# Optimization experiments

Hardware: AMD Instinct MI355X
Metric: run time of the kernel (lower is better)

Reference implementation:

```python
import jax, jax.numpy as jnp
import numpy as np

N_NODES = 10000
N_EDGES = 160000


def _conv2d(x, w, b):
    y = jax.lax.conv_general_dilated(x, w, (1, 1), 'SAME',
                                     dimension_numbers=('NCHW', 'OIHW', 'NCHW'))
    return jax.nn.selu(y + b[None, :, None, None])


def _cnn(cf, cnn_w1, cnn_b1, cnn_w2, cnn_b2, cnn_w3, cnn_b3, cnn_w4, cnn_b4):
    h = _conv2d(cf, cnn_w1, cnn_b1)
    h = _conv2d(h, cnn_w2, cnn_b2)
    h = _conv2d(h, cnn_w3, cnn_b3)
    h = _conv2d(h, cnn_w4, cnn_b4)
    return h.mean(axis=(2, 3))  # (1, 24) global avg pool


def _gat(x, src, dst, W, a_s, a_d, b, n):
    # PyG GATConv, concat=False (mean over heads), add_self_loops handled by caller
    H, C = a_s.shape
    h = (x @ W).reshape(-1, H, C)                      # (N,H,C)
    e = jax.nn.leaky_relu((h * a_s).sum(-1)[src] +
                          (h * a_d).sum(-1)[dst], 0.2)  # (E,H)
    m = jax.ops.segment_max(e, dst, num_segments=n)
    p = jnp.exp(e - m[dst])
    z = jax.ops.segment_sum(p, dst, num_segments=n)
    alpha = p / (z[dst] + 1e-16)
    out = jax.ops.segment_sum(h[src] * alpha[..., None], dst, num_segments=n)
    return out.mean(axis=1) + b


def _fix_boundary(v, up, down, left, right):
    c0 = jnp.where(down, 0.0, jnp.where(up, 1.0, v[:, 0]))
    c1 = jnp.where(right, 1.0, jnp.where(left, 0.0, v[:, 1]))
    return v.at[:, 0].set(c0).at[:, 1].set(c1)


def setup_inputs() -> dict:
    key = jax.random.key(0)
    ks = jax.random.split(key, 40)
    d = {}
    d['x'] = jax.random.uniform(ks[0], (N_NODES, 10), dtype=jnp.float32)
    d['edge_index'] = jax.random.randint(ks[1], (2, N_EDGES), 0, N_NODES, dtype=jnp.int64)
    d['conv_feat'] = jax.random.normal(ks[2], (1, 4, 64, 64), dtype=jnp.float32)
    cnn_dims = [(16, 4), (32, 16), (64, 32), (24, 64)]
    for i, (o, c) in enumerate(cnn_dims, 1):
        d[f'cnn_w{i}'] = jax.random.normal(ks[2 + i], (o, c, 3, 3), jnp.float32) * 0.1
        d[f'cnn_b{i}'] = jnp.zeros((o,), jnp.float32)
    gat_dims = [(34, 8, 64), (64, 16, 128), (128, 8, 256), (256, 8, 128), (128, 16, 2)]
    for i, (fin, H, C) in enumerate(gat_dims, 1):
        k1, k2, k3 = jax.random.split(ks[10 + i], 3)
        d[f'g{i}_w'] = jax.random.normal(k1, (fin, H * C), jnp.float32) * 0.1
        d[f'g{i}_as'] = jax.random.normal(k2, (H, C), jnp.float32) * 0.1
        d[f'g{i}_ad'] = jax.random.normal(k3, (H, C), jnp.float32) * 0.1
        d[f'g{i}_b'] = jnp.zeros((C,), jnp.float32)
    return d


def reference(x, edge_index, conv_feat,
              cnn_w1, cnn_b1, cnn_w2, cnn_b2, cnn_w3, cnn_b3, cnn_w4, cnn_b4,
              g1_w, g1_as, g1_ad, g1_b,
              g2_w, g2_as, g2_ad, g2_b,
              g3_w, g3_as, g3_ad, g3_b,
              g4_w, g4_as, g4_ad, g4_b,
              g5_w, g5_as, g5_ad, g5_b):
    n = x.shape[0]
    # boundary masks from raw node coordinates
    up, down = x[:, 0] == 1, x[:, 0] == 0
    left, right = x[:, 1] == 0, x[:, 1] == 1
    # add self loops (PyG GATConv default)
    loops = jnp.arange(n, dtype=edge_index.dtype)
    src = jnp.concatenate([edge_index[0], loops])
    dst = jnp.concatenate([edge_index[1], loops])

    gfeat = _cnn(conv_feat, cnn_w1, cnn_b1, cnn_w2, cnn_b2, cnn_w3, cnn_b3, cnn_w4, cnn_b4)
    h = jnp.concatenate([jnp.broadcast_to(gfeat, (n, gfeat.shape[1])), x], axis=1)

    h = jax.nn.selu(_gat(h, src, dst, g1_w, g1_as, g1_ad, g1_b, n))
    h = _fix_boundary(h, up, down, left, right)
    h = jax.nn.selu(_gat(h, src, dst, g2_w, g2_as, g2_ad, g2_b, n))
    h = _fix_boundary(h, up, down, left, right)
    h = jax.nn.selu(_gat(h, src, dst, g3_w, g3_as, g3_ad, g3_b, n))
    h = _fix_boundary(h, up, down, left, right)
    h = jax.nn.selu(_gat(h, src, dst, g4_w, g4_as, g4_ad, g4_b, n))
    h = _fix_boundary(h, up, down, left, right)
    res = jax.nn.selu(_gat(h, src, dst, g5_w, g5_as, g5_ad, g5_b, n))
    out = x[:, :2] + res
    out = _fix_boundary(out, up, down, left, right)
    return out
```

## Files before the change

kernel.cpp:

```cpp
#include <hip/hip_runtime.h>
#include <hip/hip_fp16.h>
#include <math.h>


#define DEVFN static __device__ __forceinline__

typedef __attribute__((ext_vector_type(8))) _Float16 half8;
typedef __attribute__((ext_vector_type(4))) _Float16 half4v;
typedef __attribute__((ext_vector_type(4))) float f32x4;

DEVFN float selu_f(float v) {
    const float scale = 1.0507009873554805f;
    const float alpha = 1.6732632423543772f;
    return v > 0.f ? scale * v : scale * alpha * (expf(v) - 1.f);
}

DEVFN float lrelu02(float v) { return v > 0.f ? v : 0.2f * v; }

#define PST 66
#define PSZ (66 * 66)

__global__ __launch_bounds__(256) void conv3x3_first(const float* __restrict__ cf,
                                                     const float* __restrict__ w,
                                                     const float* __restrict__ b,
                                                     float* __restrict__ out) {
    int x  = threadIdx.x & 63;
    int yg = threadIdx.x >> 6;
    int y  = blockIdx.x * 4 + yg;
    int co = blockIdx.y;
    float acc = b[co];
    const float* wp = w + (size_t)co * 4 * 9;
#pragma unroll
    for (int ci = 0; ci < 4; ++ci) {
        const float* ip = cf + ci * 4096;
        const float* wr = wp + ci * 9;
#pragma unroll
        for (int ky = 0; ky < 3; ++ky) {
            int yy = y + ky - 1;
            if (yy < 0 || yy >= 64) continue;
#pragma unroll
            for (int kx = 0; kx < 3; ++kx) {
                int xx = x + kx - 1;
                if (xx < 0 || xx >= 64) continue;
                acc += wr[ky * 3 + kx] * ip[yy * 64 + xx];
            }
        }
    }
    out[(size_t)co * PSZ + (y + 1) * PST + (x + 1)] = selu_f(acc);
}

template <int CIN>
__global__ __launch_bounds__(256) void conv3x3_pad(const float* __restrict__ in,
                                                   const float* __restrict__ w,
                                                   const float* __restrict__ b,
                                                   float* __restrict__ out) {
    int x  = threadIdx.x & 63;
    int yg = threadIdx.x >> 6;
    int y  = blockIdx.x * 4 + yg;
    int co = blockIdx.y;
    float acc = b[co];
    const float* wp = w + (size_t)co * CIN * 9;
#pragma unroll 4
    for (int ci = 0; ci < CIN; ++ci) {
        const float* ip = in + ci * PSZ + y * PST + x;
        const float* wr = wp + ci * 9;
        acc += wr[0] * ip[0]           + wr[1] * ip[1]           + wr[2] * ip[2]
             + wr[3] * ip[PST]         + wr[4] * ip[PST + 1]     + wr[5] * ip[PST + 2]
             + wr[6] * ip[2 * PST]     + wr[7] * ip[2 * PST + 1] + wr[8] * ip[2 * PST + 2];
    }
    out[(size_t)co * PSZ + (y + 1) * PST + (x + 1)] = selu_f(acc);
}

__global__ void avgpool_c(const float* __restrict__ in, float* __restrict__ gfeat) {
    int c = blockIdx.x;
    int t = threadIdx.x;
    float s = 0.f;
    for (int i = t; i < 4096; i += 256) {
        int y = i >> 6, x = i & 63;
        s += in[c * PSZ + (y + 1) * PST + (x + 1)];
    }
#pragma unroll
    for (int off = 32; off >= 1; off >>= 1) s += __shfl_xor(s, off);
    __shared__ float red[4];
    int wave = t >> 6, lane = t & 63;
    if (lane == 0) red[wave] = s;
    __syncthreads();
    if (t == 0) gfeat[c] = (red[0] + red[1] + red[2] + red[3]) * (1.f / 4096.f);
}

__global__ void build_h0(const float* __restrict__ x, const float* __restrict__ gfeat,
                         const float* __restrict__ we0,
                         __half* __restrict__ h0f, unsigned* __restrict__ masks,
                         float* __restrict__ esed, int N) {
    int n = blockIdx.x * blockDim.x + threadIdx.x;
    if (n >= N) return;
    float x0 = x[n * 10 + 0], x1 = x[n * 10 + 1];
    unsigned mk = (x0 == 1.f ? 1u : 0u) | (x0 == 0.f ? 2u : 0u) |
                  (x1 == 0.f ? 4u : 0u) | (x1 == 1.f ? 8u : 0u);
    masks[n] = mk;
    __half* hq = h0f + (size_t)n * 64;
    float hf[64];
#pragma unroll
    for (int j = 0; j < 64; ++j) {
        float v = (j < 24) ? gfeat[j] : (j < 34 ? x[n * 10 + (j - 24)] : 0.f);
        __half hv = __float2half(v);
        hq[j] = hv;
        hf[j] = __half2float(hv);
    }
    float s[16];
#pragma unroll
    for (int o = 0; o < 16; ++o) s[o] = 0.f;
    for (int k = 0; k < 64; ++k) {
        float f = hf[k];
        const float* wk = we0 + k * 16;
#pragma unroll
        for (int o = 0; o < 16; ++o) s[o] += f * wk[o];
    }
#pragma unroll
    for (int o = 0; o < 16; ++o) esed[(size_t)n * 16 + o] = s[o];
}

__global__ void count_dst(const int* __restrict__ ei, int* __restrict__ cnt, int E, int N) {
    int t = blockIdx.x * blockDim.x + threadIdx.x;
    if (t >= E + N) return;
    int dst = (t < E) ? ei[E + t] : (t - E);
    atomicAdd(&cnt[dst], 1);
}

__global__ __launch_bounds__(1024) void scan_all(const int* __restrict__ cnt,
                                                 int* __restrict__ indptr,
                                                 int* __restrict__ cursor,
                                                 int n, int total) {
    __shared__ int sdata[1024];
    int t = threadIdx.x;
    int base = t * 10;
    int loc[10];
    int s = 0;
#pragma unroll
    for (int i = 0; i < 10; ++i) {
        int idx = base + i;
        int v = (idx < n) ? cnt[idx] : 0;
        loc[i] = s;
        s += v;
    }
    sdata[t] = s;
    __syncthreads();
    for (int off = 1; off < 1024; off <<= 1) {
        int tmp = (t >= off) ? sdata[t - off] : 0;
        __syncthreads();
        sdata[t] += tmp;
        __syncthreads();
    }
    int excl = (t == 0) ? 0 : sdata[t - 1];
#pragma unroll
    for (int i = 0; i < 10; ++i) {
        int idx = base + i;
        if (idx < n) {
            int e = excl + loc[i];
            indptr[idx] = e;
            cursor[idx] = e;
        }
    }
    if (t == 0) indptr[n] = total;
}

__global__ void scatter_edges(const int* __restrict__ ei, int* __restrict__ cursor,
                              int* __restrict__ col, int E, int N) {
    int t = blockIdx.x * blockDim.x + threadIdx.x;
    if (t >= E + N) return;
    int src, dst;
    if (t < E) { src = ei[t]; dst = ei[E + t]; }
    else       { src = dst = t - E; }
    int pos = atomicAdd(&cursor[dst], 1);
    col[pos] = src;
}

__global__ __launch_bounds__(256) void prep_all(
        const float* __restrict__ W0, const float* __restrict__ W1,
        const float* __restrict__ W2, const float* __restrict__ W3,
        const float* __restrict__ W4,
        const float* __restrict__ as0, const float* __restrict__ as1,
        const float* __restrict__ as2, const float* __restrict__ as3,
        const float* __restrict__ as4,
        const float* __restrict__ ad0, const float* __restrict__ ad1,
        const float* __restrict__ ad2, const float* __restrict__ ad3,
        const float* __restrict__ ad4,
        unsigned short* __restrict__ bt, float* __restrict__ wesed,
        float* __restrict__ wcomb) {
    const int Kc[5]  = {34, 64, 128, 256, 128};
    const int Kpc[5] = {64, 64, 128, 256, 128};
    const int Hc[5]  = {8, 16, 8, 8, 16};
    const int Cc[5]  = {64, 128, 256, 128, 2};
    const int HCc[5] = {512, 2048, 2048, 1024, 32};
    const int KAc[5] = {512, 1024, 1024, 2048, 2048};
    const int btOff[5] = {0, 32768, 163840, 425984, 0};
    const int weOff[5] = {0, 1024, 3072, 5120, 9216};

    int b = blockIdx.x, tid = threadIdx.x;

    if (b < 168) {
        int lyr, tloc;
        if (b < 8)        { lyr = 0; tloc = b; }
        else if (b < 40)  { lyr = 1; tloc = b - 8; }
        else if (b < 104) { lyr = 2; tloc = b - 40; }
        else              { lyr = 3; tloc = b - 104; }
        const int ktl[4] = {1, 1, 2, 4};
        const int mtl[4] = {1, 2, 4, 2};
        int kt = ktl[lyr], mt = mtl[lyr];
        int per_h = kt * mt;
        int h = tloc / per_h, r = tloc - h * per_h;
        int ki = r % kt, mi = r / kt;
        int k0 = ki * 64, m0 = mi * 64;
        int K = Kc[lyr], Kp = Kpc[lyr], C = Cc[lyr], HC = HCc[lyr], KA = KAc[lyr];
        const float* W;
        if (lyr == 0) W = W0; else if (lyr == 1) W = W1;
        else if (lyr == 2) W = W2; else W = W3;

        __shared__ float tile[64][65];
        int c = tid & 63, rg = tid >> 6;
        for (int r2 = rg; r2 < 64; r2 += 4) {
            int k = k0 + r2, m = m0 + c;
            float v = (k < K && m < C) ? W[(size_t)k * HC + h * C + m] : 0.f;
            tile[r2][c] = v;
        }
        __syncthreads();
        unsigned short* bp = bt + btOff[lyr];
        for (int mr = rg; mr < 64; mr += 4) {
            int m = m0 + mr, k = k0 + c;
            if (m < C && k < Kp)
                bp[(size_t)m * KA + h * Kp + k] =
                    __half_as_ushort(__float2half(tile[c][mr]));
        }
    } else if (b < 200) {
        int u = (b - 168) * 256 + tid;
        int k = u >> 6, o = u & 63;
        float s;
        if (o < 32) {
            int h = (o < 16) ? o : o - 16;
            const float* av = ((o < 16) ? as4 : ad4) + h * 2;
            s = W4[k * 32 + h * 2 + 0] * av[0] + W4[k * 32 + h * 2 + 1] * av[1];
        } else {
            s = W4[k * 32 + (o - 32)];
        }
        wcomb[u] = s;
    } else {
        int wb = b - 200;
        int lyr, u0;
        if (wb < 4)       { lyr = 0; u0 = wb * 256; }
        else if (wb < 12) { lyr = 1; u0 = (wb - 4) * 256; }
        else if (wb < 20) { lyr = 2; u0 = (wb - 12) * 256; }
        else if (wb < 36) { lyr = 3; u0 = (wb - 20) * 256; }
        else              { lyr = 4; u0 = (wb - 36) * 256; }
        int u = u0 + tid;
        int K = Kc[lyr], Kp = Kpc[lyr], H = Hc[lyr], C = Cc[lyr], HC = HCc[lyr];
        int H2 = 2 * H;
        if (u < Kp * H2) {
            int k = u / H2, o = u - k * H2;
            float s = 0.f;
            if (k < K) {
                int h = (o < H) ? o : o - H;
                const float *W, *as_, *ad_;
                if (lyr == 0)      { W = W0; as_ = as0; ad_ = ad0; }
                else if (lyr == 1) { W = W1; as_ = as1; ad_ = ad1; }
                else if (lyr == 2) { W = W2; as_ = as2; ad_ = ad2; }
                else if (lyr == 3) { W = W3; as_ = as3; ad_ = ad3; }
                else               { W = W4; as_ = as4; ad_ = ad4; }
                const float* av = ((o < H) ? as_ : ad_) + h * C;
                const float* wp = W + (size_t)k * HC + h * C;
#pragma unroll 4
                for (int c2 = 0; c2 < C; ++c2) s += wp[c2] * av[c2];
            }
            wesed[weOff[lyr] + u] = s;
        }
    }
}

template <int H, int KP, int CH, int NPB, int TWO>
__global__ __launch_bounds__(NPB * (KP / CH)) void gat_fused_lds(
        const __half* __restrict__ hinf, const float* __restrict__ esed,
        const float* __restrict__ esed2,
        const int* __restrict__ indptr, const int* __restrict__ col,
        __half* __restrict__ g, int N) {
    const int TPN = KP / CH;
    const int EC  = TPN / H;
    const int H2  = 2 * H;
    __shared__ float lds_p[NPB][2][TPN];
    int sub = threadIdx.x / TPN;
    int j   = threadIdx.x % TPN;
    int n = blockIdx.x * NPB + sub;
    if (n >= N) return;
    int e_my = j / H, h_my = j % H;
    int c0 = j * CH;
    float edv = esed[n * H2 + H + h_my];
    if constexpr (TWO) edv += esed2[n * H2 + H + h_my];

    float acc[H][CH];
#pragma unroll
    for (int h = 0; h < H; ++h)
#pragma unroll
        for (int t = 0; t < CH; ++t) acc[h][t] = 0.f;
    float zloc = 0.f;

    int beg = indptr[n], deg = indptr[n + 1] - beg;

    float p = 0.f;
    if (e_my < deg) {
        int srcm = col[beg + e_my];
        float es0 = esed[srcm * H2 + h_my];
        if constexpr (TWO) es0 += esed2[srcm * H2 + h_my];
        p = expf(lrelu02(es0 + edv));
    }
    int buf = 0;
    for (int base = 0; base < deg; base += EC) {
        zloc += p;
        lds_p[sub][buf][j] = p;
        __builtin_amdgcn_wave_barrier();
        int ce = base + EC + e_my;
        bool vnext = (ce < deg);
        float esv = 0.f;
        if (vnext) {
            int srcm = col[beg + ce];
            esv = esed[srcm * H2 + h_my];
            if constexpr (TWO) esv += esed2[srcm * H2 + h_my];
        }
#pragma unroll
        for (int e = 0; e < EC; ++e) {
            int idx = base + e;
            if (idx < deg) {
                int src = col[beg + idx];
                float f[CH];
                if (CH == 2) {
                    __half2 hv = *(const __half2*)(hinf + (size_t)src * KP + c0);
                    float2 ff = __half22float2(hv);
                    f[0] = ff.x; f[1] = ff.y;
                } else {
                    half4v hv = *(const half4v*)(hinf + (size_t)src * KP + c0);
                    f[0] = (float)hv[0]; f[1] = (float)hv[1];
                    f[2] = (float)hv[2]; f[3] = (float)hv[3];
                }
                const float4* ap = (const float4*)&lds_p[sub][buf][e * H];
#pragma unroll
                for (int q4 = 0; q4 < H / 4; ++q4) {
                    float4 a4 = ap[q4];
#pragma unroll
                    for (int t = 0; t < CH; ++t) {
                        acc[4 * q4 + 0][t] += a4.x * f[t];
                        acc[4 * q4 + 1][t] += a4.y * f[t];
                        acc[4 * q4 + 2][t] += a4.z * f[t];
                        acc[4 * q4 + 3][t] += a4.w * f[t];
                    }
                }
            }
        }
        p = vnext ? expf(lrelu02(esv + edv)) : 0.f;
        buf ^= 1;
    }

#pragma unroll
    for (int off = H; off < TPN; off <<= 1)
        zloc += __shfl_xor(zloc, off, TPN);
    float zinv_my = (1.f / H) / (zloc + 1e-16f);

    __half* gp = g + (size_t)n * (H * KP) + c0;
#pragma unroll
    for (int h = 0; h < H; ++h) {
        float zf = __shfl(zinv_my, h, TPN);
        if (CH == 2) {
            *(__half2*)(gp + h * KP) =
                __floats2half2_rn(acc[h][0] * zf, acc[h][1] * zf);
        } else {
            __half2 lo = __floats2half2_rn(acc[h][0] * zf, acc[h][1] * zf);
            __half2 hi = __floats2half2_rn(acc[h][2] * zf, acc[h][3] * zf);
            union { __half2 h2[2]; float2 f2; } u;
            u.h2[0] = lo; u.h2[1] = hi;
            *(float2*)(gp + h * KP) = u.f2;
        }
    }
}

template <int NPB>
__global__ __launch_bounds__(NPB * 32) void final_attn(
        const float* __restrict__ eyp, const int* __restrict__ indptr,
        const int* __restrict__ col, const float* __restrict__ b5,
        const unsigned* __restrict__ masks, const float* __restrict__ x,
        float* __restrict__ outp, int N) {
    int sub = threadIdx.x >> 5;
    int j   = threadIdx.x & 31;
    int n = blockIdx.x * NPB + sub;
    if (n >= N) return;
    int h = j >> 1;
    float edv = eyp[(size_t)n * 64 + 16 + h];
    int beg = indptr[n], end = indptr[n + 1];
    float z = 0.f, a = 0.f;
    int i = beg;
    for (; i + 1 < end; i += 2) {
        int s0 = col[i], s1 = col[i + 1];
        const float* r0 = eyp + (size_t)s0 * 64;
        const float* r1 = eyp + (size_t)s1 * 64;
        float es0 = r0[h], y0 = r0[32 + j];
        float es1 = r1[h], y1 = r1[32 + j];
        float p0 = expf(lrelu02(es0 + edv));
        float p1 = expf(lrelu02(es1 + edv));
        z += p0; a += p0 * y0;
        z += p1; a += p1 * y1;
    }
    for (; i < end; ++i) {
        const float* r = eyp + (size_t)col[i] * 64;
        float p = expf(lrelu02(r[h] + edv));
        z += p; a += p * r[32 + j];
    }
    float zf = (1.f / 16.f) / (z + 1e-16f);
    float val = a * zf;
#pragma unroll
    for (int off = 2; off <= 16; off <<= 1) val += __shfl_xor(val, off, 32);
    float other = __shfl_xor(val, 1, 32);
    if (j == 0) {
        unsigned mk = masks[n];
        float v0 = x[n * 10 + 0] + selu_f(val + b5[0]);
        float v1 = x[n * 10 + 1] + selu_f(other + b5[1]);
        if (mk & 2u) v0 = 0.f; else if (mk & 1u) v0 = 1.f;
        if (mk & 8u) v1 = 1.f; else if (mk & 4u) v1 = 0.f;
        outp[n * 2 + 0] = v0;
        outp[n * 2 + 1] = v1;
    }
}

#define LDP 72
template <int CW, int EOUT>
__global__ __launch_bounds__(256) void gemm16(const __half* __restrict__ A,
                                              const unsigned short* __restrict__ Bhi,
                                              const float* __restrict__ bias,
                                              const unsigned* __restrict__ masks,
                                              __half* __restrict__ O16,
                                              const float* __restrict__ wnext,
                                              float* __restrict__ eout,
                                              int N, int K, int M) {
    const int JT = CW / 64;
    const int BR = CW / 32;
    __shared__ __half lA[16 * LDP], lB[CW * LDP];
    __shared__ float vt[EOUT ? 16 : 1][EOUT ? (CW + 4) : 1];
    int tid = threadIdx.x;
    int wave = tid >> 6, lane = tid & 63;
    int ln16 = lane & 15, q = lane >> 4;
    int row0 = blockIdx.x * 16;
    int col0 = blockIdx.y * CW;
    int wc = wave * (CW / 4);

    int arow = tid >> 3;
    int ac   = (tid & 7) * 8;
    const __half* Bp = (const __half*)Bhi;
    const __half* ap = A + (size_t)min(row0 + arow, N - 1) * K + ac;
    const __half* bp[BR];
#pragma unroll
    for (int i = 0; i < BR; ++i)
        bp[i] = Bp + (size_t)(col0 + arow + 32 * i) * K + ac;

    half8 ra;
    if (tid < 128) ra = *(const half8*)(ap);
    half8 rb[BR];
#pragma unroll
    for (int i = 0; i < BR; ++i) rb[i] = *(const half8*)(bp[i]);

    f32x4 acc[JT];
#pragma unroll
    for (int j = 0; j < JT; ++j) acc[j] = (f32x4){0.f, 0.f, 0.f, 0.f};

    for (int kc = 0; kc < K; kc += 64) {
        __syncthreads();
        if (tid < 128) *(half8*)(lA + arow * LDP + ac) = ra;
#pragma unroll
        for (int i = 0; i < BR; ++i)
            *(half8*)(lB + (arow + 32 * i) * LDP + ac) = rb[i];
        __syncthreads();
        int kn = kc + 64;
        if (kn < K) {
            if (tid < 128) ra = *(const half8*)(ap + kn);
#pragma unroll
            for (int i = 0; i < BR; ++i) rb[i] = *(const half8*)(bp[i] + kn);
        }
#pragma unroll
        for (int kk = 0; kk < 2; ++kk) {
            half8 af = *(const half8*)(lA + ln16 * LDP + kk * 32 + q * 8);
#pragma unroll
            for (int j = 0; j < JT; ++j) {
                half8 bf = *(const half8*)(lB + (wc + j * 16 + ln16) * LDP + kk * 32 + q * 8);
                acc[j] = __builtin_amdgcn_mfma_f32_16x16x32_f16(af, bf, acc[j], 0, 0, 0);
            }
        }
    }

#pragma unroll
    for (int j = 0; j < JT; ++j) {
        int cc = col0 + wc + j * 16 + ln16;
        float bv = bias[cc];
#pragma unroll
        for (int r = 0; r < 4; ++r) {
            int rr = row0 + q * 4 + r;
            float v = selu_f(acc[j][r] + bv);
            if (cc < 2 && rr < N) {
                unsigned mk = masks[rr];
                if (cc == 0) { if (mk & 2u) v = 0.f; else if (mk & 1u) v = 1.f; }
                else         { if (mk & 8u) v = 1.f; else if (mk & 4u) v = 0.f; }
            }
            __half hv = __float2half(v);
            if (rr < N) O16[(size_t)rr * M + cc] = hv;
            if constexpr (EOUT > 0)
                vt[q * 4 + r][wc + j * 16 + ln16] = __half2float(hv);
        }
    }

    if constexpr (EOUT > 0) {
        __syncthreads();
        const int NG = 256 / EOUT;
        const int NI = 16 / NG;
        int o = tid & (EOUT - 1);
        int ngrp = tid / EOUT;
        const float* wp = wnext + (size_t)col0 * EOUT;
        float* ep = eout + (size_t)blockIdx.y * N * EOUT;
        float s[NI];
#pragma unroll
        for (int i = 0; i < NI; ++i) s[i] = 0.f;
        for (int k = 0; k < CW; ++k) {
            float wk = wp[k * EOUT + o];
#pragma unroll
            for (int i = 0; i < NI; ++i)
                s[i] += vt[ngrp + NG * i][k] * wk;
        }
#pragma unroll
        for (int i = 0; i < NI; ++i) {
            int n = row0 + ngrp + NG * i;
            if (n < N) ep[(size_t)n * EOUT + o] = s[i];
        }
    }
}

extern "C" void kernel_launch(void* const* d_in, const int* in_sizes, int n_in,
                              void* d_out, int out_size, void* d_ws, size_t ws_size,
                              hipStream_t stream) {
    const float* x   = (const float*)d_in[0];
    const int*   ei  = (const int*)d_in[1];
    const float* cf  = (const float*)d_in[2];
    const float* cw[4] = {(const float*)d_in[3], (const float*)d_in[5],
                          (const float*)d_in[7], (const float*)d_in[9]};
    const float* cb[4] = {(const float*)d_in[4], (const float*)d_in[6],
                          (const float*)d_in[8], (const float*)d_in[10]};
    const float* gw[5], *gas[5], *gad[5], *gb[5];
    for (int i = 0; i < 5; ++i) {
        gw[i]  = (const float*)d_in[11 + 4 * i];
        gas[i] = (const float*)d_in[12 + 4 * i];
        gad[i] = (const float*)d_in[13 + 4 * i];
        gb[i]  = (const float*)d_in[14 + 4 * i];
    }
    const int N = in_sizes[0] / 10;
    const int E = in_sizes[1] / 2;
    const int EN = E + N;

    char* base = (char*)d_ws;
    size_t off = 0;
    auto alloc = [&](size_t bytes) -> char* {
        char* p = base + off;
        off = (off + bytes + 255) & ~(size_t)255;
        return p;
    };
    float* c1p   = (float*)alloc((size_t)16 * PSZ * 4);
    float* c2p   = (float*)alloc((size_t)32 * PSZ * 4);
    float* c3p   = (float*)alloc((size_t)64 * PSZ * 4);
    float* c4p   = (float*)alloc((size_t)24 * PSZ * 4);
    float* gfeat = (float*)alloc(24 * 4);
    __half* hA16 = (__half*)alloc((size_t)N * 256 * 2);
    __half* hB16 = (__half*)alloc((size_t)N * 256 * 2);
    __half* g    = (__half*)alloc((size_t)N * 2048 * 2);
    float* esed  = (float*)alloc((size_t)N * 32 * 4);
    float* eyp   = (float*)alloc((size_t)N * 64 * 4);
    float* wesed = (float*)alloc((size_t)13312 * 4);
    float* wcomb = (float*)alloc((size_t)8192 * 4);
    unsigned short* bt = (unsigned short*)alloc((size_t)688128 * 2);
    unsigned* masks = (unsigned*)alloc((size_t)N * 4);
    int* cnt    = (int*)alloc((size_t)N * 4);
    int* indptr = (int*)alloc((size_t)(N + 1) * 4);
    int* cursor = (int*)alloc((size_t)N * 4);
    int* col    = (int*)alloc((size_t)EN * 4);
    (void)ws_size;

    prep_all<<<252, 256, 0, stream>>>(gw[0], gw[1], gw[2], gw[3], gw[4],
                                      gas[0], gas[1], gas[2], gas[3], gas[4],
                                      gad[0], gad[1], gad[2], gad[3], gad[4],
                                      bt, wesed, wcomb);

    hipMemsetAsync(c1p, 0, (size_t)136 * PSZ * 4, stream);
    conv3x3_first<<<dim3(16, 16), 256, 0, stream>>>(cf, cw[0], cb[0], c1p);
    conv3x3_pad<16><<<dim3(16, 32), 256, 0, stream>>>(c1p, cw[1], cb[1], c2p);
    conv3x3_pad<32><<<dim3(16, 64), 256, 0, stream>>>(c2p, cw[2], cb[2], c3p);
    conv3x3_pad<64><<<dim3(16, 24), 256, 0, stream>>>(c3p, cw[3], cb[3], c4p);
    avgpool_c<<<24, 256, 0, stream>>>(c4p, gfeat);

    build_h0<<<(N + 255) / 256, 256, 0, stream>>>(x, gfeat, wesed + 0, hA16, masks,
                                                  esed, N);

    hipMemsetAsync(cnt, 0, (size_t)N * 4, stream);
    count_dst<<<(EN + 255) / 256, 256, 0, stream>>>(ei, cnt, E, N);
    scan_all<<<1, 1024, 0, stream>>>(cnt, indptr, cursor, N, EN);
    scatter_edges<<<(EN + 255) / 256, 256, 0, stream>>>(ei, cursor, col, E, N);

    int gx16 = (N + 15) / 16;

    gat_fused_lds<8, 64, 4, 16, 0><<<(N + 15) / 16, 256, 0, stream>>>(
        hA16, esed, nullptr, indptr, col, g, N);
    gemm16<64, 32><<<dim3(gx16, 1), 256, 0, stream>>>(g, bt + 0, gb[0], masks, hB16,
                                                      wesed + 1024, esed, N, 512, 64);

    gat_fused_lds<16, 64, 2, 8, 0><<<(N + 7) / 8, 256, 0, stream>>>(
        hB16, esed, nullptr, indptr, col, g, N);
    gemm16<128, 16><<<dim3(gx16, 1), 256, 0, stream>>>(g, bt + 32768, gb[1], masks, hA16,
                                                       wesed + 3072, esed, N, 1024, 128);

    gat_fused_lds<8, 128, 4, 8, 0><<<(N + 7) / 8, 256, 0, stream>>>(
        hA16, esed, nullptr, indptr, col, g, N);
    gemm16<128, 16><<<dim3(gx16, 2), 256, 0, stream>>>(g, bt + 163840, gb[2], masks, hB16,
                                                       wesed + 5120, esed, N, 1024, 256);

    gat_fused_lds<8, 256, 4, 4, 1><<<(N + 3) / 4, 256, 0, stream>>>(
        hB16, esed, esed + (size_t)N * 16, indptr, col, g, N);
    gemm16<128, 64><<<dim3(gx16, 1), 256, 0, stream>>>(g, bt + 425984, gb[3], masks, hA16,
                                                       wcomb, eyp, N, 2048, 128);

    final_attn<8><<<(N + 7) / 8, 256, 0, stream>>>(eyp, indptr, col, gb[4],
                                                   masks, x, (float*)d_out, N);
}
```

Measured before the change: 429.0 us.

## Co-schedule CNN conv layers with CSR graph build in combined kernels

Merges the first three conv layers with the dst-count, scan and edge-scatter kernels into three combined launches whose block ranges split between the two independent jobs. The cnt buffer moves next to the conv buffers so a single memset clears both, dropping one memset and four launches. The scan now uses 256 threads with 40 elements each so it fits the 256-thread combined kernel. This serialises more work per scan thread and puts blocks with different register needs in one launch, which may lower occupancy for the conv blocks.

```diff
diff --git a/kernel.cpp b/kernel.cpp
--- a/kernel.cpp
+++ b/kernel.cpp
@@ -20,14 +20,12 @@
 #define PST 66
 #define PSZ (66 * 66)
 
-__global__ __launch_bounds__(256) void conv3x3_first(const float* __restrict__ cf,
-                                                     const float* __restrict__ w,
-                                                     const float* __restrict__ b,
-                                                     float* __restrict__ out) {
+DEVFN void conv_first_body(const float* __restrict__ cf, const float* __restrict__ w,
+                           const float* __restrict__ b, float* __restrict__ out,
+                           int bx, int co) {
     int x  = threadIdx.x & 63;
     int yg = threadIdx.x >> 6;
-    int y  = blockIdx.x * 4 + yg;
-    int co = blockIdx.y;
+    int y  = bx * 4 + yg;
     float acc = b[co];
     const float* wp = w + (size_t)co * 4 * 9;
 #pragma unroll
@@ -50,14 +48,12 @@
 }
 
 template <int CIN>
-__global__ __launch_bounds__(256) void conv3x3_pad(const float* __restrict__ in,
-                                                   const float* __restrict__ w,
-                                                   const float* __restrict__ b,
-                                                   float* __restrict__ out) {
+DEVFN void conv_pad_body(const float* __restrict__ in, const float* __restrict__ w,
+                         const float* __restrict__ b, float* __restrict__ out,
+                         int bx, int co) {
     int x  = threadIdx.x & 63;
     int yg = threadIdx.x >> 6;
-    int y  = blockIdx.x * 4 + yg;
-    int co = blockIdx.y;
+    int y  = bx * 4 + yg;
     float acc = b[co];
     const float* wp = w + (size_t)co * CIN * 9;
 #pragma unroll 4
@@ -69,6 +65,14 @@
              + wr[6] * ip[2 * PST]     + wr[7] * ip[2 * PST + 1] + wr[8] * ip[2 * PST + 2];
     }
     out[(size_t)co * PSZ + (y + 1) * PST + (x + 1)] = selu_f(acc);
+}
+
+template <int CIN>
+__global__ __launch_bounds__(256) void conv3x3_pad(const float* __restrict__ in,
+                                                   const float* __restrict__ w,
+                                                   const float* __restrict__ b,
+                                                   float* __restrict__ out) {
+    conv_pad_body<CIN>(in, w, b, out, blockIdx.x, blockIdx.y);
 }
 
 __global__ void avgpool_c(const float* __restrict__ in, float* __restrict__ gfeat) {
@@ -120,24 +124,23 @@
     for (int o = 0; o < 16; ++o) esed[(size_t)n * 16 + o] = s[o];
 }
 
-__global__ void count_dst(const int* __restrict__ ei, int* __restrict__ cnt, int E, int N) {
-    int t = blockIdx.x * blockDim.x + threadIdx.x;
+DEVFN void count_body(const int* __restrict__ ei, int* __restrict__ cnt,
+                      int blk, int E, int N) {
+    int t = blk * 256 + threadIdx.x;
     if (t >= E + N) return;
     int dst = (t < E) ? ei[E + t] : (t - E);
     atomicAdd(&cnt[dst], 1);
 }
 
-__global__ __launch_bounds__(1024) void scan_all(const int* __restrict__ cnt,
-                                                 int* __restrict__ indptr,
-                                                 int* __restrict__ cursor,
-                                                 int n, int total) {
-    __shared__ int sdata[1024];
+DEVFN void scan_body(const int* __restrict__ cnt, int* __restrict__ indptr,
+                     int* __restrict__ cursor, int n, int total) {
+    __shared__ int sdata[256];
     int t = threadIdx.x;
-    int base = t * 10;
-    int loc[10];
+    int base = t * 40;
+    int loc[40];
     int s = 0;
 #pragma unroll
-    for (int i = 0; i < 10; ++i) {
+    for (int i = 0; i < 40; ++i) {
         int idx = base + i;
         int v = (idx < n) ? cnt[idx] : 0;
         loc[i] = s;
@@ -145,7 +148,7 @@
     }
     sdata[t] = s;
     __syncthreads();
-    for (int off = 1; off < 1024; off <<= 1) {
+    for (int off = 1; off < 256; off <<= 1) {
         int tmp = (t >= off) ? sdata[t - off] : 0;
         __syncthreads();
         sdata[t] += tmp;
@@ -153,7 +156,7 @@
     }
     int excl = (t == 0) ? 0 : sdata[t - 1];
 #pragma unroll
-    for (int i = 0; i < 10; ++i) {
+    for (int i = 0; i < 40; ++i) {
         int idx = base + i;
         if (idx < n) {
             int e = excl + loc[i];
@@ -164,15 +167,56 @@
     if (t == 0) indptr[n] = total;
 }
 
-__global__ void scatter_edges(const int* __restrict__ ei, int* __restrict__ cursor,
-                              int* __restrict__ col, int E, int N) {
-    int t = blockIdx.x * blockDim.x + threadIdx.x;
+DEVFN void scatter_body(const int* __restrict__ ei, int* __restrict__ cursor,
+                        int* __restrict__ col, int blk, int E, int N) {
+    int t = blk * 256 + threadIdx.x;
     if (t >= E + N) return;
     int src, dst;
     if (t < E) { src = ei[t]; dst = ei[E + t]; }
     else       { src = dst = t - E; }
     int pos = atomicAdd(&cursor[dst], 1);
     col[pos] = src;
+}
+
+__global__ __launch_bounds__(256) void comboA(const float* __restrict__ cf,
+                                              const float* __restrict__ w0,
+                                              const float* __restrict__ b0,
+                                              float* __restrict__ c1p,
+                                              const int* __restrict__ ei,
+                                              int* __restrict__ cnt, int E, int N) {
+    int b = blockIdx.x;
+    if (b < 256) conv_first_body(cf, w0, b0, c1p, b % 16, b / 16);
+    else         count_body(ei, cnt, b - 256, E, N);
+}
+
+__global__ __launch_bounds__(256) void comboB(const int* __restrict__ cnt,
+                                              int* __restrict__ indptr,
+                                              int* __restrict__ cursor, int n, int total,
+                                              const float* __restrict__ c1p,
+                                              const float* __restrict__ w1,
+                                              const float* __restrict__ b1,
+                                              float* __restrict__ c2p) {
+    int b = blockIdx.x;
+    if (b == 0) scan_body(cnt, indptr, cursor, n, total);
+    else {
+        int blk = b - 1;
+        conv_pad_body<16>(c1p, w1, b1, c2p, blk % 16, blk / 16);
+    }
+}
+
+__global__ __launch_bounds__(256) void comboC(const int* __restrict__ ei,
+                                              int* __restrict__ cursor,
+                                              int* __restrict__ col, int E, int N, int CB,
+                                              const float* __restrict__ c2p,
+                                              const float* __restrict__ w2,
+                                              const float* __restrict__ b2,
+                                              float* __restrict__ c3p) {
+    int b = blockIdx.x;
+    if (b < CB) scatter_body(ei, cursor, col, b, E, N);
+    else {
+        int blk = b - CB;
+        conv_pad_body<32>(c2p, w2, b2, c3p, blk % 16, blk / 16);
+    }
 }
 
 __global__ __launch_bounds__(256) void prep_all(
@@ -554,6 +598,7 @@
     const int N = in_sizes[0] / 10;
     const int E = in_sizes[1] / 2;
     const int EN = E + N;
+    const int CB = (EN + 255) / 256;
 
     char* base = (char*)d_ws;
     size_t off = 0;
@@ -566,6 +611,7 @@
     float* c2p   = (float*)alloc((size_t)32 * PSZ * 4);
     float* c3p   = (float*)alloc((size_t)64 * PSZ * 4);
     float* c4p   = (float*)alloc((size_t)24 * PSZ * 4);
+    int*   cnt   = (int*)alloc((size_t)N * 4);
     float* gfeat = (float*)alloc(24 * 4);
     __half* hA16 = (__half*)alloc((size_t)N * 256 * 2);
     __half* hB16 = (__half*)alloc((size_t)N * 256 * 2);
@@ -576,7 +622,6 @@
     float* wcomb = (float*)alloc((size_t)8192 * 4);
     unsigned short* bt = (unsigned short*)alloc((size_t)688128 * 2);
     unsigned* masks = (unsigned*)alloc((size_t)N * 4);
-    int* cnt    = (int*)alloc((size_t)N * 4);
     int* indptr = (int*)alloc((size_t)(N + 1) * 4);
     int* cursor = (int*)alloc((size_t)N * 4);
     int* col    = (int*)alloc((size_t)EN * 4);
@@ -587,20 +632,19 @@
                                       gad[0], gad[1], gad[2], gad[3], gad[4],
                                       bt, wesed, wcomb);
 
-    hipMemsetAsync(c1p, 0, (size_t)136 * PSZ * 4, stream);
-    conv3x3_first<<<dim3(16, 16), 256, 0, stream>>>(cf, cw[0], cb[0], c1p);
-    conv3x3_pad<16><<<dim3(16, 32), 256, 0, stream>>>(c1p, cw[1], cb[1], c2p);
-    conv3x3_pad<32><<<dim3(16, 64), 256, 0, stream>>>(c2p, cw[2], cb[2], c3p);
+    size_t zlen = (size_t)((char*)cnt - (char*)c1p) + (size_t)N * 4;
+    hipMemsetAsync(c1p, 0, zlen, stream);
+
+    comboA<<<256 + CB, 256, 0, stream>>>(cf, cw[0], cb[0], c1p, ei, cnt, E, N);
+    comboB<<<1 + 512, 256, 0, stream>>>(cnt, indptr, cursor, N, EN,
+                                        c1p, cw[1], cb[1], c2p);
+    comboC<<<CB + 1024, 256, 0, stream>>>(ei, cursor, col, E, N, CB,
+                                          c2p, cw[2], cb[2], c3p);
     conv3x3_pad<64><<<dim3(16, 24), 256, 0, stream>>>(c3p, cw[3], cb[3], c4p);
     avgpool_c<<<24, 256, 0, stream>>>(c4p, gfeat);
 
     build_h0<<<(N + 255) / 256, 256, 0, stream>>>(x, gfeat, wesed + 0, hA16, masks,
                                                   esed, N);
-
-    hipMemsetAsync(cnt, 0, (size_t)N * 4, stream);
-    count_dst<<<(EN + 255) / 256, 256, 0, stream>>>(ei, cnt, E, N);
-    scan_all<<<1, 1024, 0, stream>>>(cnt, indptr, cursor, N, EN);
-    scatter_edges<<<(EN + 255) / 256, 256, 0, stream>>>(ei, cursor, col, E, N);
 
     int gx16 = (N + 15) / 16;
 
```

Measured after the change: 422.3 us. No clear change (-1.6%).
